# Kernel tuning notes

Measured on AMD Instinct MI355X. Metric: run time of the kernel, lower is better.

## Reference

```python
import jax, jax.numpy as jnp
import numpy as np

NBASE = 4                       # number of bases (DNA)
NSTATE = 2 * NBASE * (NBASE + 1)  # = 40 flip-flop transition states
SCALE = 5.0
LARGE_LOG_VAL = 50000.0


def setup_inputs() -> dict:
    key = jax.random.key(0)
    kx, kw, kb = jax.random.split(key, 3)
    T, N, INSIZE = 2048, 128, 256
    x = jax.random.normal(kx, (T, N, INSIZE), dtype=jnp.float32)
    # orthonormal-ish init approximated by scaled gaussian
    W = jax.random.normal(kw, (NSTATE, INSIZE), dtype=jnp.float32) / np.float32(np.sqrt(INSIZE))
    b = 0.5 * jax.random.normal(kb, (NSTATE,), dtype=jnp.float32)
    return {"x": x, "W": W, "b": b}


def _log_partition_flipflop(scores):
    """Forward-algorithm log partition function. scores: (T, N, C)."""
    T, N, C = scores.shape
    fwd0 = jnp.concatenate(
        [jnp.zeros((N, NBASE), scores.dtype),
         jnp.full((N, NBASE), -LARGE_LOG_VAL, scores.dtype)], axis=1)
    logZ0 = jax.nn.logsumexp(fwd0, axis=1, keepdims=True)  # (N, 1)
    fwd0 = fwd0 - logZ0

    def step(carry, scores_t):
        fwd, logZ = carry
        # (N, nbase+1, 2*nbase): to-state grouped transition scores
        curr = fwd[:, None, :] + scores_t.reshape(N, NBASE + 1, 2 * NBASE)
        base1 = jax.nn.logsumexp(curr[:, :NBASE], axis=2)            # (N, nbase) flip states
        base2 = jnp.logaddexp(curr[:, NBASE, :NBASE],
                              curr[:, NBASE, NBASE:])               # (N, nbase) flop states
        new_state = jnp.concatenate([base1, base2], axis=1)          # (N, 2*nbase)
        factors = jax.nn.logsumexp(new_state, axis=1, keepdims=True)  # (N, 1)
        return (new_state - factors, logZ + factors), None

    (_, logZ), _ = jax.lax.scan(step, (fwd0, logZ0), scores)
    return logZ  # (N, 1)


def reference(x, W, b):
    T = x.shape[0]
    # scale * tanh(x W^T + b) -> transition scores (T, N, NSTATE)
    y = SCALE * jnp.tanh(jnp.einsum('tni,ci->tnc', x, W) + b)
    logZ = _log_partition_flipflop(y)          # (N, 1)
    return y - logZ / np.float32(T)            # broadcast over T and C
```

## Files before the change

kernel.cpp:

```cpp
#include <hip/hip_runtime.h>
#include <hip/hip_bf16.h>

#define T_DIM 2048
#define N_DIM 128
#define K_DIM 256
#define C_DIM 40
#define SEG 256
#define SEGLEN 8
#define GRP 8
#define SEGPERGRP 32

typedef __attribute__((ext_vector_type(8))) short bf16x8;
typedef __attribute__((ext_vector_type(4))) float f32x4v;

__device__ __forceinline__ unsigned pack_bf16(float a, float b) {
    union { float f; unsigned u; } ua, ub;
    ua.f = a; ub.f = b;
    unsigned ra = (ua.u + 0x7FFFu + ((ua.u >> 16) & 1u)) >> 16;
    unsigned rb = (ub.u + 0x7FFFu + ((ub.u >> 16) & 1u)) >> 16;
    return (ra & 0xFFFFu) | (rb << 16);
}

__device__ __forceinline__ float fast_tanh(float v) {
    float e = __expf(2.f * v);
    return 1.f - 2.f / (e + 1.f);
}

__global__ __launch_bounds__(256) void k_gemm_tanh(
    const float* __restrict__ x, const float* __restrict__ W,
    const float* __restrict__ b, float* __restrict__ y)
{
    __shared__ __align__(16) unsigned shW[6144];
    __shared__ __align__(16) float shX[4][2][4096];

    const int tid = threadIdx.x;

    for (int i = tid; i < 6144; i += 256) {
        int flat = i * 2;
        int r = flat >> 8;
        int k = flat & 255;
        float v0 = 0.f, v1 = 0.f;
        if (r < C_DIM) { v0 = W[r * K_DIM + k]; v1 = W[r * K_DIM + k + 1]; }
        int byte = (k * 2) ^ ((r & 7) << 4);
        shW[(r * 512 + byte) >> 2] = pack_bf16(v0, v1);
    }
    __syncthreads();

    const int lane = tid & 63;
    const int wave = tid >> 6;
    const int lr = lane & 15;
    const int kg = lane >> 4;
    const int gw = blockIdx.x * 4 + wave;
    const int bswz = (lr & 7) << 4;
    const char* cW = reinterpret_cast<const char*>(shW);

    float4 bia0 = *reinterpret_cast<const float4*>(b + kg * 4);
    float4 bia1 = *reinterpret_cast<const float4*>(b + 16 + kg * 4);
    float4 bia2 = {0.f, 0.f, 0.f, 0.f};
    if (kg < 2) bia2 = *reinterpret_cast<const float4*>(b + 32 + kg * 4);

    auto stage = [&](int tile, int buf) {
        const char* gbase = reinterpret_cast<const char*>(x) + (size_t)tile * 16 * 1024;
        float* lbase = &shX[wave][buf][0];
        #pragma unroll
        for (int r = 0; r < 16; ++r) {
            int srcoff = (lane * 16) ^ ((r & 7) << 4);
            const void* gp = gbase + r * 1024 + srcoff;
            __builtin_amdgcn_global_load_lds(
                (const __attribute__((address_space(1))) void*)gp,
                (__attribute__((address_space(3))) void*)(lbase + r * 256),
                16, 0, 0);
        }
    };

    stage(gw * 16, 0);

    for (int tt = 0; tt < 16; ++tt) {
        int cur = tt & 1;
        if (tt < 15) stage(gw * 16 + tt + 1, cur ^ 1);
        __builtin_amdgcn_sched_barrier(0);
        if (tt < 15) asm volatile("s_waitcnt vmcnt(16)" ::: "memory");
        else         asm volatile("s_waitcnt vmcnt(0)" ::: "memory");
        __builtin_amdgcn_sched_barrier(0);

        const char* cX = reinterpret_cast<const char*>(&shX[wave][cur][0]);
        f32x4v acc0 = {0.f, 0.f, 0.f, 0.f};
        f32x4v acc1 = {0.f, 0.f, 0.f, 0.f};
        f32x4v acc2 = {0.f, 0.f, 0.f, 0.f};

        #pragma unroll
        for (int kt = 0; kt < 8; ++kt) {
            int g = kg * 32 + kt * 128;
            float4 d0 = *reinterpret_cast<const float4*>(cX + lr * 1024 + (g ^ bswz));
            float4 d1 = *reinterpret_cast<const float4*>(cX + lr * 1024 + ((g + 16) ^ bswz));
            union { bf16x8 v; unsigned u[4]; } xf;
            xf.u[0] = pack_bf16(d0.x, d0.y);
            xf.u[1] = pack_bf16(d0.z, d0.w);
            xf.u[2] = pack_bf16(d1.x, d1.y);
            xf.u[3] = pack_bf16(d1.z, d1.w);

            int kb2 = kt * 64 + kg * 16;
            bf16x8 a0 = *reinterpret_cast<const bf16x8*>(cW + lr * 512 + (kb2 ^ bswz));
            bf16x8 a1 = *reinterpret_cast<const bf16x8*>(cW + (16 + lr) * 512 + (kb2 ^ bswz));
            bf16x8 a2 = *reinterpret_cast<const bf16x8*>(cW + (32 + lr) * 512 + (kb2 ^ bswz));
            acc0 = __builtin_amdgcn_mfma_f32_16x16x32_bf16(a0, xf.v, acc0, 0, 0, 0);
            acc1 = __builtin_amdgcn_mfma_f32_16x16x32_bf16(a1, xf.v, acc1, 0, 0, 0);
            acc2 = __builtin_amdgcn_mfma_f32_16x16x32_bf16(a2, xf.v, acc2, 0, 0, 0);
        }

        size_t row = (size_t)(gw * 16 + tt) * 16 + lr;
        float* yr = y + row * C_DIM;
        float4 o0, o1;
        o0.x = 5.f * fast_tanh(acc0[0] + bia0.x);
        o0.y = 5.f * fast_tanh(acc0[1] + bia0.y);
        o0.z = 5.f * fast_tanh(acc0[2] + bia0.z);
        o0.w = 5.f * fast_tanh(acc0[3] + bia0.w);
        o1.x = 5.f * fast_tanh(acc1[0] + bia1.x);
        o1.y = 5.f * fast_tanh(acc1[1] + bia1.y);
        o1.z = 5.f * fast_tanh(acc1[2] + bia1.z);
        o1.w = 5.f * fast_tanh(acc1[3] + bia1.w);
        *reinterpret_cast<float4*>(yr + kg * 4) = o0;
        *reinterpret_cast<float4*>(yr + 16 + kg * 4) = o1;
        if (kg < 2) {
            float4 o2;
            o2.x = 5.f * fast_tanh(acc2[0] + bia2.x);
            o2.y = 5.f * fast_tanh(acc2[1] + bia2.y);
            o2.z = 5.f * fast_tanh(acc2[2] + bia2.z);
            o2.w = 5.f * fast_tanh(acc2[3] + bia2.w);
            *reinterpret_cast<float4*>(yr + 32 + kg * 4) = o2;
        }
    }
}

__global__ __launch_bounds__(128) void k_seg(
    const float* __restrict__ y, float* __restrict__ segv, float* __restrict__ segl)
{
    int tid = blockIdx.x * 128 + threadIdx.x;
    int n = tid & 127;
    int s = tid >> 7;

    float P[8][8];
    #pragma unroll
    for (int j = 0; j < 8; ++j)
        #pragma unroll
        for (int c = 0; c < 8; ++c) P[j][c] = (j == c) ? 1.f : 0.f;

    for (int st = 0; st < SEGLEN; ++st) {
        int t = s * SEGLEN + st;
        const float* yr = y + ((size_t)t * N_DIM + n) * C_DIM;
        float e[40];
        #pragma unroll
        for (int i = 0; i < 10; ++i) {
            float4 v = reinterpret_cast<const float4*>(yr)[i];
            e[i * 4 + 0] = __expf(v.x);
            e[i * 4 + 1] = __expf(v.y);
            e[i * 4 + 2] = __expf(v.z);
            e[i * 4 + 3] = __expf(v.w);
        }
        #pragma unroll
        for (int c = 0; c < 8; ++c) {
            float np[8];
            #pragma unroll
            for (int j = 0; j < 4; ++j) {
                float a = 0.f;
                #pragma unroll
                for (int i = 0; i < 8; ++i) a += P[i][c] * e[j * 8 + i];
                np[j] = a;
            }
            #pragma unroll
            for (int j = 0; j < 4; ++j)
                np[4 + j] = P[j][c] * e[32 + j] + P[4 + j][c] * e[36 + j];
            #pragma unroll
            for (int j = 0; j < 8; ++j) P[j][c] = np[j];
        }
    }
    #pragma unroll
    for (int c = 0; c < 8; ++c) {
        float sum = 0.f;
        #pragma unroll
        for (int j = 0; j < 8; ++j) sum += P[j][c];
        float inv = 1.f / sum;
        #pragma unroll
        for (int j = 0; j < 8; ++j)
            segv[(((size_t)s * 8 + c) * 8 + j) * N_DIM + n] = P[j][c] * inv;
        segl[((size_t)s * 8 + c) * N_DIM + n] = __logf(sum);
    }
}

__global__ __launch_bounds__(256) void k_grp(
    const float* __restrict__ segv, const float* __restrict__ segl,
    float* __restrict__ grpv, float* __restrict__ grpl)
{
    int tid = blockIdx.x * 256 + threadIdx.x;
    int n = tid & 127;
    int cc = (tid >> 7) & 7;
    int g = tid >> 10;

    float u[8];
    #pragma unroll
    for (int i = 0; i < 8; ++i) u[i] = (i == cc) ? 1.f : 0.f;
    float logacc = 0.f;

    for (int s = g * SEGPERGRP; s < (g + 1) * SEGPERGRP; ++s) {
        float l[8];
        #pragma unroll
        for (int i = 0; i < 8; ++i) l[i] = segl[((size_t)s * 8 + i) * N_DIM + n];
        float m = l[0];
        #pragma unroll
        for (int i = 1; i < 8; ++i) m = fmaxf(m, l[i]);
        float nu[8] = {0.f, 0.f, 0.f, 0.f, 0.f, 0.f, 0.f, 0.f};
        #pragma unroll
        for (int i = 0; i < 8; ++i) {
            float wi = u[i] * __expf(l[i] - m);
            #pragma unroll
            for (int j = 0; j < 8; ++j)
                nu[j] += wi * segv[(((size_t)s * 8 + i) * 8 + j) * N_DIM + n];
        }
        float sum = 0.f;
        #pragma unroll
        for (int j = 0; j < 8; ++j) sum += nu[j];
        float inv = 1.f / sum;
        #pragma unroll
        for (int j = 0; j < 8; ++j) u[j] = nu[j] * inv;
        logacc += m + __logf(sum);
    }
    #pragma unroll
    for (int j = 0; j < 8; ++j)
        grpv[(((size_t)g * 8 + cc) * 8 + j) * N_DIM + n] = u[j];
    grpl[((size_t)g * 8 + cc) * N_DIM + n] = logacc;
}

__global__ void k_fin(const float* __restrict__ grpv, const float* __restrict__ grpl,
                      float* __restrict__ lz)
{
    int n = threadIdx.x;
    float p[8] = {0.25f, 0.25f, 0.25f, 0.25f, 0.f, 0.f, 0.f, 0.f};
    float logZ = 1.3862943611198906f;

    for (int g = 0; g < GRP; ++g) {
        float l[8];
        #pragma unroll
        for (int i = 0; i < 8; ++i) l[i] = grpl[((size_t)g * 8 + i) * N_DIM + n];
        float m = l[0];
        #pragma unroll
        for (int i = 1; i < 8; ++i) m = fmaxf(m, l[i]);
        float nu[8] = {0.f, 0.f, 0.f, 0.f, 0.f, 0.f, 0.f, 0.f};
        #pragma unroll
        for (int i = 0; i < 8; ++i) {
            float wi = p[i] * __expf(l[i] - m);
            #pragma unroll
            for (int j = 0; j < 8; ++j)
                nu[j] += wi * grpv[(((size_t)g * 8 + i) * 8 + j) * N_DIM + n];
        }
        float sum = 0.f;
        #pragma unroll
        for (int j = 0; j < 8; ++j) sum += nu[j];
        float inv = 1.f / sum;
        #pragma unroll
        for (int j = 0; j < 8; ++j) p[j] = nu[j] * inv;
        logZ += m + __logf(sum);
    }
    lz[n] = logZ * (1.f / (float)T_DIM);
}

__global__ __launch_bounds__(256) void k_sub(float* __restrict__ out,
                                             const float* __restrict__ lz)
{
    int i = blockIdx.x * 256 + threadIdx.x;
    int n = (i / 10) & 127;
    float d = lz[n];
    float4* o = reinterpret_cast<float4*>(out) + i;
    float4 v = *o;
    v.x -= d; v.y -= d; v.z -= d; v.w -= d;
    *o = v;
}

extern "C" void kernel_launch(void* const* d_in, const int* in_sizes, int n_in,
                              void* d_out, int out_size, void* d_ws, size_t ws_size,
                              hipStream_t stream) {
    const float* x = (const float*)d_in[0];
    const float* W = (const float*)d_in[1];
    const float* b = (const float*)d_in[2];
    float* out = (float*)d_out;
    float* ws = (float*)d_ws;

    float* segv = ws;
    float* segl = ws + 2097152;
    float* grpv = ws + 2359296;
    float* grpl = ws + 2424832;
    float* lz   = ws + 2433024;

    k_gemm_tanh<<<256, 256, 0, stream>>>(x, W, b, out);
    k_seg<<<256, 128, 0, stream>>>(out, segv, segl);
    k_grp<<<32, 256, 0, stream>>>(segv, segl, grpv, grpl);
    k_fin<<<1, 128, 0, stream>>>(grpv, grpl, lz);
    k_sub<<<10240, 256, 0, stream>>>(out, lz);
}
```

Baseline: 147.7 us.

## Keep W fragments in registers, halve LDS staging, and double the GEMM grid

The GEMM+tanh kernel no longer stages W in shared memory. Each lane loads its bf16 W fragments straight into registers. The x staging is split into two half-K buffers per wave that are refilled as each half is consumed, which halves shared memory per block. The grid is doubled with launch_bounds(256,2) so each wave handles 8 tiles instead of 16. The aim is higher occupancy and more memory parallelism for this bandwidth-bound GEMM, at the cost of 24 bf16x8 registers per lane and finer-grained vmcnt synchronisation.

```diff
diff --git a/kernel.cpp b/kernel.cpp
--- a/kernel.cpp
+++ b/kernel.cpp
@@ -26,89 +26,106 @@
     return 1.f - 2.f / (e + 1.f);
 }
 
-__global__ __launch_bounds__(256) void k_gemm_tanh(
+__global__ __launch_bounds__(256, 2) void k_gemm_tanh(
     const float* __restrict__ x, const float* __restrict__ W,
     const float* __restrict__ b, float* __restrict__ y)
 {
-    __shared__ __align__(16) unsigned shW[6144];
-    __shared__ __align__(16) float shX[4][2][4096];
+    __shared__ __align__(16) float shX[4][2][16][128];
 
     const int tid = threadIdx.x;
-
-    for (int i = tid; i < 6144; i += 256) {
-        int flat = i * 2;
-        int r = flat >> 8;
-        int k = flat & 255;
-        float v0 = 0.f, v1 = 0.f;
-        if (r < C_DIM) { v0 = W[r * K_DIM + k]; v1 = W[r * K_DIM + k + 1]; }
-        int byte = (k * 2) ^ ((r & 7) << 4);
-        shW[(r * 512 + byte) >> 2] = pack_bf16(v0, v1);
-    }
-    __syncthreads();
-
     const int lane = tid & 63;
     const int wave = tid >> 6;
     const int lr = lane & 15;
     const int kg = lane >> 4;
     const int gw = blockIdx.x * 4 + wave;
-    const int bswz = (lr & 7) << 4;
-    const char* cW = reinterpret_cast<const char*>(shW);
+    const int t0 = gw * 8;
+    const int aswz = (lr & 7) << 4;
+
+    bf16x8 wf[3][8];
+    #pragma unroll
+    for (int cb = 0; cb < 3; ++cb) {
+        #pragma unroll
+        for (int kk = 0; kk < 8; ++kk) {
+            int rowc = cb * 16 + lr;
+            float4 w0 = {0.f, 0.f, 0.f, 0.f}, w1 = {0.f, 0.f, 0.f, 0.f};
+            if (rowc < C_DIM) {
+                const float* wp = W + rowc * K_DIM + kg * 8 + kk * 32;
+                w0 = *reinterpret_cast<const float4*>(wp);
+                w1 = *reinterpret_cast<const float4*>(wp + 4);
+            }
+            union { bf16x8 v; unsigned u[4]; } uw;
+            uw.u[0] = pack_bf16(w0.x, w0.y);
+            uw.u[1] = pack_bf16(w0.z, w0.w);
+            uw.u[2] = pack_bf16(w1.x, w1.y);
+            uw.u[3] = pack_bf16(w1.z, w1.w);
+            wf[cb][kk] = uw.v;
+        }
+    }
 
     float4 bia0 = *reinterpret_cast<const float4*>(b + kg * 4);
     float4 bia1 = *reinterpret_cast<const float4*>(b + 16 + kg * 4);
     float4 bia2 = {0.f, 0.f, 0.f, 0.f};
     if (kg < 2) bia2 = *reinterpret_cast<const float4*>(b + 32 + kg * 4);
 
-    auto stage = [&](int tile, int buf) {
-        const char* gbase = reinterpret_cast<const char*>(x) + (size_t)tile * 16 * 1024;
-        float* lbase = &shX[wave][buf][0];
-        #pragma unroll
-        for (int r = 0; r < 16; ++r) {
-            int srcoff = (lane * 16) ^ ((r & 7) << 4);
-            const void* gp = gbase + r * 1024 + srcoff;
+    auto stage = [&](int h) {
+        int tile = t0 + (h >> 1);
+        const char* gbase = reinterpret_cast<const char*>(x)
+                          + (size_t)tile * 16384 + (h & 1) * 512;
+        float* lbase = &shX[wave][h & 1][0][0];
+        #pragma unroll
+        for (int j = 0; j < 8; ++j) {
+            int r = 2 * j + (lane >> 5);
+            int off = ((lane & 31) * 16) ^ ((r & 7) << 4);
+            const void* gp = gbase + r * 1024 + off;
             __builtin_amdgcn_global_load_lds(
                 (const __attribute__((address_space(1))) void*)gp,
-                (__attribute__((address_space(3))) void*)(lbase + r * 256),
+                (__attribute__((address_space(3))) void*)(lbase + j * 256),
                 16, 0, 0);
         }
     };
 
-    stage(gw * 16, 0);
-
-    for (int tt = 0; tt < 16; ++tt) {
-        int cur = tt & 1;
-        if (tt < 15) stage(gw * 16 + tt + 1, cur ^ 1);
-        __builtin_amdgcn_sched_barrier(0);
-        if (tt < 15) asm volatile("s_waitcnt vmcnt(16)" ::: "memory");
-        else         asm volatile("s_waitcnt vmcnt(0)" ::: "memory");
-        __builtin_amdgcn_sched_barrier(0);
-
-        const char* cX = reinterpret_cast<const char*>(&shX[wave][cur][0]);
-        f32x4v acc0 = {0.f, 0.f, 0.f, 0.f};
-        f32x4v acc1 = {0.f, 0.f, 0.f, 0.f};
-        f32x4v acc2 = {0.f, 0.f, 0.f, 0.f};
-
-        #pragma unroll
-        for (int kt = 0; kt < 8; ++kt) {
-            int g = kg * 32 + kt * 128;
-            float4 d0 = *reinterpret_cast<const float4*>(cX + lr * 1024 + (g ^ bswz));
-            float4 d1 = *reinterpret_cast<const float4*>(cX + lr * 1024 + ((g + 16) ^ bswz));
-            union { bf16x8 v; unsigned u[4]; } xf;
-            xf.u[0] = pack_bf16(d0.x, d0.y);
-            xf.u[1] = pack_bf16(d0.z, d0.w);
-            xf.u[2] = pack_bf16(d1.x, d1.y);
-            xf.u[3] = pack_bf16(d1.z, d1.w);
-
-            int kb2 = kt * 64 + kg * 16;
-            bf16x8 a0 = *reinterpret_cast<const bf16x8*>(cW + lr * 512 + (kb2 ^ bswz));
-            bf16x8 a1 = *reinterpret_cast<const bf16x8*>(cW + (16 + lr) * 512 + (kb2 ^ bswz));
-            bf16x8 a2 = *reinterpret_cast<const bf16x8*>(cW + (32 + lr) * 512 + (kb2 ^ bswz));
-            acc0 = __builtin_amdgcn_mfma_f32_16x16x32_bf16(a0, xf.v, acc0, 0, 0, 0);
-            acc1 = __builtin_amdgcn_mfma_f32_16x16x32_bf16(a1, xf.v, acc1, 0, 0, 0);
-            acc2 = __builtin_amdgcn_mfma_f32_16x16x32_bf16(a2, xf.v, acc2, 0, 0, 0);
-        }
-
-        size_t row = (size_t)(gw * 16 + tt) * 16 + lr;
+    f32x4v acc0, acc1, acc2;
+
+#define COMPUTE_HALF(KH)                                                          \
+    do {                                                                          \
+        const char* cX = reinterpret_cast<const char*>(&shX[wave][KH][0][0]);     \
+        _Pragma("unroll")                                                         \
+        for (int kt = 0; kt < 4; ++kt) {                                          \
+            int k0 = kg * 32 + kt * 128;                                          \
+            float4 d0 = *reinterpret_cast<const float4*>(cX + lr * 512 + (k0 ^ aswz));        \
+            float4 d1 = *reinterpret_cast<const float4*>(cX + lr * 512 + ((k0 + 16) ^ aswz)); \
+            union { bf16x8 v; unsigned u[4]; } xf;                                \
+            xf.u[0] = pack_bf16(d0.x, d0.y);                                      \
+            xf.u[1] = pack_bf16(d0.z, d0.w);                                      \
+            xf.u[2] = pack_bf16(d1.x, d1.y);                                      \
+            xf.u[3] = pack_bf16(d1.z, d1.w);                                      \
+            acc0 = __builtin_amdgcn_mfma_f32_16x16x32_bf16(wf[0][KH * 4 + kt], xf.v, acc0, 0, 0, 0); \
+            acc1 = __builtin_amdgcn_mfma_f32_16x16x32_bf16(wf[1][KH * 4 + kt], xf.v, acc1, 0, 0, 0); \
+            acc2 = __builtin_amdgcn_mfma_f32_16x16x32_bf16(wf[2][KH * 4 + kt], xf.v, acc2, 0, 0, 0); \
+        }                                                                         \
+    } while (0)
+
+    stage(0);
+    stage(1);
+
+    for (int t = 0; t < 8; ++t) {
+        __builtin_amdgcn_sched_barrier(0);
+        asm volatile("s_waitcnt vmcnt(8)" ::: "memory");
+        __builtin_amdgcn_sched_barrier(0);
+        acc0 = (f32x4v){0.f, 0.f, 0.f, 0.f};
+        acc1 = (f32x4v){0.f, 0.f, 0.f, 0.f};
+        acc2 = (f32x4v){0.f, 0.f, 0.f, 0.f};
+        COMPUTE_HALF(0);
+        __builtin_amdgcn_sched_barrier(0);
+        if (t < 7) stage(2 * t + 2);
+
+        __builtin_amdgcn_sched_barrier(0);
+        if (t < 7) asm volatile("s_waitcnt vmcnt(8)" ::: "memory");
+        else       asm volatile("s_waitcnt vmcnt(0)" ::: "memory");
+        __builtin_amdgcn_sched_barrier(0);
+        COMPUTE_HALF(1);
+
+        size_t row = (size_t)(t0 + t) * 16 + lr;
         float* yr = y + row * C_DIM;
         float4 o0, o1;
         o0.x = 5.f * fast_tanh(acc0[0] + bia0.x);
@@ -129,7 +146,11 @@
             o2.w = 5.f * fast_tanh(acc2[3] + bia2.w);
             *reinterpret_cast<float4*>(yr + 32 + kg * 4) = o2;
         }
-    }
+
+        __builtin_amdgcn_sched_barrier(0);
+        if (t < 7) stage(2 * t + 3);
+    }
+#undef COMPUTE_HALF
 }
 
 __global__ __launch_bounds__(128) void k_seg(
@@ -290,7 +311,7 @@
     float* grpl = ws + 2424832;
     float* lz   = ws + 2433024;
 
-    k_gemm_tanh<<<256, 256, 0, stream>>>(x, W, b, out);
+    k_gemm_tanh<<<512, 256, 0, stream>>>(x, W, b, out);
     k_seg<<<256, 128, 0, stream>>>(out, segv, segl);
     k_grp<<<32, 256, 0, stream>>>(segv, segl, grpv, grpl);
     k_fin<<<1, 128, 0, stream>>>(grpv, grpl, lz);
```

Measured after the change: 148.5 us. No clear change (+0.5%).
